# Kernel tuning notes

Hardware: AMD Instinct MI355X
Metric: run time of the kernel (lower is better)

Reference implementation:

```python
import jax, jax.numpy as jnp
import numpy as np

N = 1048576
N_GRID = 256
DX = 1.0 / N_GRID
INV_DX = float(N_GRID)
DT = 2e-5
P_VOL = (DX * 0.5) ** 2
P_RHO = 1.0
P_MASS = P_VOL * P_RHO
E_MOD = 1000.0
NU = 0.2
MU_0 = E_MOD / (2.0 * (1.0 + NU))
LAM_0 = E_MOD * NU / ((1.0 + NU) * (1.0 - 2.0 * NU))
GRAVITY = 50.0


def setup_inputs() -> dict:
    key = jax.random.key(0)
    k = jax.random.split(key, 5)
    x = 0.1 + 0.8 * jax.random.uniform(k[0], (N, 2), dtype=jnp.float32)
    v = 0.1 * jax.random.normal(k[1], (N, 2), dtype=jnp.float32)
    C = 0.5 * jax.random.normal(k[2], (N, 2, 2), dtype=jnp.float32)
    F = jnp.eye(2, dtype=jnp.float32)[None] + 0.1 * jax.random.normal(k[3], (N, 2, 2), dtype=jnp.float32)
    material = jax.random.randint(k[4], (N,), 0, 3, dtype=jnp.int32)
    Jp = jnp.ones((N,), dtype=jnp.float32)
    return {"x": x, "v": v, "C": C, "F": F, "material": material, "Jp": Jp}


def reference(x, v, C, F, material, Jp):
    dt, inv_dx, dx = DT, INV_DX, DX
    base = jnp.floor(x * inv_dx - 0.5).astype(jnp.int32)          # [N,2]
    fx = x * inv_dx - base.astype(x.dtype)                        # [N,2]
    # quadratic B-spline weights, stacked over the 3 taps -> [3,N,2]
    w = jnp.stack([0.5 * (1.5 - fx) ** 2,
                   0.75 - (fx - 1.0) ** 2,
                   0.5 * (fx - 0.5) ** 2], axis=0)

    # deformation gradient update
    F = F + dt * jnp.einsum('nij,njk->nik', C, F)

    h = jnp.exp(10.0 * (1.0 - Jp))
    h = jnp.where(material == 1, 0.3, h)
    mu = jnp.where(material == 0, 0.0, MU_0 * h)
    lam = LAM_0 * h

    # per-particle 2x2 SVD (original pads to 3x3 and slices back)
    U, sig, Vh = jnp.linalg.svd(F)

    # snow plasticity: clamp singular values, track Jp
    clamped = jnp.clip(sig, 1.0 - 2.5e-2, 1.0 + 4.5e-3)
    is_snow = material == 2
    Jp = jnp.where(is_snow, Jp * jnp.prod(sig / clamped, axis=-1), Jp)
    sig = jnp.where(is_snow[:, None], clamped, sig)

    J = jnp.prod(sig, axis=-1)
    eye2 = jnp.eye(2, dtype=x.dtype)
    F_fluid = eye2[None] * jnp.sqrt(J)[:, None, None]             # J^(1/n_dim), n_dim=2
    F_snow = jnp.einsum('nij,nj,njk->nik', U, sig, Vh)
    F = jnp.where((material == 0)[:, None, None], F_fluid,
                  jnp.where(is_snow[:, None, None], F_snow, F))

    R = jnp.einsum('nij,njk->nik', U, Vh)
    stress = (2.0 * mu[:, None, None] * jnp.einsum('nij,nkj->nik', F - R, F)
              + eye2[None] * (lam * J * (J - 1.0))[:, None, None])
    stress = (-dt * P_VOL * 4.0 * inv_dx ** 2) * stress
    affine = stress + P_MASS * C                                   # [N,2,2]

    # ---- P2G scatter over the 3x3 stencil (vectorized over 9 taps) ----
    offs = jnp.array([[i, j] for i in range(3) for j in range(3)], dtype=jnp.int32)  # [9,2]
    weight = w[offs[:, 0], :, 0] * w[offs[:, 1], :, 1]             # [9,N]
    target = base[None, :, :] + offs[:, None, :]                   # [9,N,2]
    idx = target[..., 0] * N_GRID + target[..., 1]                 # [9,N]
    flat_idx = idx.reshape(-1)
    NG2 = N_GRID * N_GRID

    v_add = P_MASS * v - jnp.einsum('nij,nj->ni', affine, x)       # [N,2]
    grid_v = jax.ops.segment_sum((weight[..., None] * v_add[None]).reshape(-1, 2),
                                 flat_idx, num_segments=NG2).reshape(N_GRID, N_GRID, 2)
    grid_affine = jax.ops.segment_sum((weight[..., None, None] * affine[None]).reshape(-1, 4),
                                      flat_idx, num_segments=NG2).reshape(N_GRID, N_GRID, 2, 2)
    grid_m = jax.ops.segment_sum((weight * P_MASS).reshape(-1),
                                 flat_idx, num_segments=NG2).reshape(N_GRID, N_GRID)

    grid_x = jnp.stack(jnp.meshgrid(jnp.arange(N_GRID), jnp.arange(N_GRID), indexing='ij'),
                       axis=-1).astype(x.dtype) * dx               # [G,G,2]
    grid_v = grid_v + jnp.einsum('abij,abj->abi', grid_affine, grid_x)

    # grid ops: momentum -> velocity, gravity, boundary clamps
    m = grid_m[..., None]
    grid_v = jnp.where(m > 0, grid_v / jnp.maximum(m, 1e-12), grid_v)
    grid_v = grid_v.at[:, :, 1].add(-dt * GRAVITY)
    grid_v = grid_v.at[:3, :, 0].max(0.0)
    grid_v = grid_v.at[-2:, :, 0].min(0.0)
    grid_v = grid_v.at[:, :3, 1].max(0.0)
    grid_v = grid_v.at[:, -2:, 1].min(0.0)

    # ---- G2P gather ----
    gvf = grid_v.reshape(NG2, 2)
    g_v = gvf[idx]                                                 # [9,N,2]
    new_v = jnp.sum(weight[..., None] * g_v, axis=0)               # [N,2]
    pos = target.astype(x.dtype) * dx                              # [9,N,2]
    new_C = jnp.sum(weight[..., None, None] * g_v[..., :, None] * pos[..., None, :], axis=0)
    new_C = (new_C - new_v[..., None] * x[:, None, :]) * (4.0 * inv_dx ** 2)

    x = x + dt * new_v
    return (x, new_v, new_C, F, material, Jp)
```

## Files before the change

kernel.cpp:

```cpp
#include <hip/hip_runtime.h>

#define NG 256
#define NG2 (NG*NG)

constexpr float DX      = 1.0f / 256.0f;
constexpr float INV_DX  = 256.0f;
constexpr float DT      = 2e-5f;
constexpr float P_VOL   = (1.0f/512.0f) * (1.0f/512.0f);
constexpr float P_MASS  = P_VOL;
constexpr float MU_0    = 1000.0f / (2.0f * 1.2f);
constexpr float LAM_0   = 1000.0f * 0.2f / (1.2f * 0.6f);
constexpr float GRAV    = 50.0f;

__device__ __forceinline__ int bin_of(float px, float py) {
    int bx = (int)floorf(px * INV_DX - 0.5f);
    int by = (int)floorf(py * INV_DX - 0.5f);
    bx = min(max(bx, 0), NG - 1);
    by = min(max(by, 0), NG - 1);
    return (bx << 8) | by;
}

__device__ __forceinline__ float bw(float t) {
    float at = fabsf(t);
    float a  = fmaxf(1.5f - at, 0.0f);
    float w1 = 0.75f - t * t;
    float w2 = 0.5f * a * a;
    return (at < 0.5f) ? w1 : w2;
}


__global__ __launch_bounds__(256) void binrank_kernel(
    const float* __restrict__ x, int* __restrict__ counts, int* __restrict__ rank, int n)
{
    int i = blockIdx.x * blockDim.x + threadIdx.x;
    if (i >= n) return;
    float2 p = ((const float2*)x)[i];
    int b = bin_of(p.x, p.y);
    rank[i] = atomicAdd(&counts[b], 1);
}

__global__ __launch_bounds__(256) void scan1_kernel(
    const int* __restrict__ counts, int* __restrict__ starts, int* __restrict__ bsum)
{
    __shared__ int tmp[256];
    int t = threadIdx.x, b = blockIdx.x;
    int v = counts[b * 256 + t];
    tmp[t] = v;
    __syncthreads();
    #pragma unroll
    for (int off = 1; off < 256; off <<= 1) {
        int add = (t >= off) ? tmp[t - off] : 0;
        __syncthreads();
        tmp[t] += add;
        __syncthreads();
    }
    starts[b * 256 + t] = tmp[t] - v;
    if (t == 255) bsum[b] = tmp[255];
}

__global__ __launch_bounds__(256) void scan2_kernel(int* __restrict__ bsum)
{
    __shared__ int tmp[256];
    int t = threadIdx.x;
    int v = bsum[t];
    tmp[t] = v;
    __syncthreads();
    #pragma unroll
    for (int off = 1; off < 256; off <<= 1) {
        int add = (t >= off) ? tmp[t - off] : 0;
        __syncthreads();
        tmp[t] += add;
        __syncthreads();
    }
    bsum[t] = tmp[t] - v;
}

__global__ __launch_bounds__(256) void scan3_kernel(
    int* __restrict__ starts, const int* __restrict__ bsum, int n)
{
    int i = blockIdx.x * blockDim.x + threadIdx.x;
    if (i < NG2) starts[i] += bsum[i >> 8];
    if (i == 0) starts[NG2] = n;
}


__device__ __forceinline__ void particle_update(
    int i,
    const float2* __restrict__ x2, const float2* __restrict__ v2,
    const float4* __restrict__ C4, const float4* __restrict__ F4,
    const int* __restrict__ mat, const float* __restrict__ Jp,
    const int* __restrict__ starts, const int* __restrict__ rank,
    float4* __restrict__ srec0, float4* __restrict__ srec1,
    float4* __restrict__ F_out4, float* __restrict__ mat_out, float* __restrict__ Jp_out)
{
    float2 xp = x2[i];
    float2 vp = v2[i];
    float4 Cp = C4[i];
    float4 Fp = F4[i];
    int    m  = mat[i];
    float  jp = Jp[i];

    float px = xp.x, py = xp.y;
    float C00 = Cp.x, C01 = Cp.y, C10 = Cp.z, C11 = Cp.w;
    float a = Fp.x, b = Fp.y, c = Fp.z, d = Fp.w;

    float na = a + DT*(C00*a + C01*c);
    float nb = b + DT*(C00*b + C01*d);
    float nc = c + DT*(C10*a + C11*c);
    float nd = d + DT*(C10*b + C11*d);
    a = na; b = nb; c = nc; d = nd;

    float h = expf(10.0f * (1.0f - jp));
    if (m == 1) h = 0.3f;
    float mu  = (m == 0) ? 0.0f : MU_0 * h;
    float lam = LAM_0 * h;

    float S00 = a*a + c*c, S01 = a*b + c*d, S11 = b*b + d*d;
    float mh = 0.5f*(S00 + S11), dh = 0.5f*(S00 - S11);
    float delta = sqrtf(dh*dh + S01*S01);
    float sig1 = sqrtf(fmaxf(mh + delta, 0.0f));
    float sig2 = sqrtf(fmaxf(mh - delta, 0.0f));
    float e0, e1;
    if (dh >= 0.0f) { e0 = delta + dh; e1 = S01; }
    else            { e0 = S01;        e1 = delta - dh; }
    float elen = sqrtf(e0*e0 + e1*e1);
    float vc, vs;
    if (elen > 1e-30f) { float il = 1.0f/elen; vc = e0*il; vs = e1*il; }
    else               { vc = 1.0f; vs = 0.0f; }
    float inv1 = 1.0f / fmaxf(sig1, 1e-30f);
    float inv2 = 1.0f / fmaxf(sig2, 1e-30f);
    float u1x = ( a*vc + b*vs) * inv1, u1y = ( c*vc + d*vs) * inv1;
    float u2x = (-a*vs + b*vc) * inv2, u2y = (-c*vs + d*vc) * inv2;

    if (m == 2) {
        float c1 = fminf(fmaxf(sig1, 1.0f - 2.5e-2f), 1.0f + 4.5e-3f);
        float c2 = fminf(fmaxf(sig2, 1.0f - 2.5e-2f), 1.0f + 4.5e-3f);
        jp = jp * (sig1 / c1) * (sig2 / c2);
        sig1 = c1; sig2 = c2;
    }
    float J = sig1 * sig2;

    if (m == 0) {
        float s = sqrtf(J);
        a = s; b = 0.0f; c = 0.0f; d = s;
    } else if (m == 2) {
        a = sig1*u1x*vc - sig2*u2x*vs;
        b = sig1*u1x*vs + sig2*u2x*vc;
        c = sig1*u1y*vc - sig2*u2y*vs;
        d = sig1*u1y*vs + sig2*u2y*vc;
    }
    float R00 = u1x*vc - u2x*vs, R01 = u1x*vs + u2x*vc;
    float R10 = u1y*vc - u2y*vs, R11 = u1y*vs + u2y*vc;

    float k2mu = 2.0f * mu;
    float fr00 = a - R00, fr01 = b - R01, fr10 = c - R10, fr11 = d - R11;
    float ljj  = lam * J * (J - 1.0f);
    float st00 = k2mu*(fr00*a + fr01*b) + ljj;
    float st01 = k2mu*(fr00*c + fr01*d);
    float st10 = k2mu*(fr10*a + fr11*b);
    float st11 = k2mu*(fr10*c + fr11*d) + ljj;
    const float coef = -DT * P_VOL * 4.0f * INV_DX * INV_DX;
    float A00 = coef*st00 + P_MASS*C00;
    float A01 = coef*st01 + P_MASS*C01;
    float A10 = coef*st10 + P_MASS*C10;
    float A11 = coef*st11 + P_MASS*C11;

    float bx_ = P_MASS*vp.x - (A00*px + A01*py);
    float by_ = P_MASS*vp.y - (A10*px + A11*py);

    int bidx = bin_of(px, py);
    int sidx = starts[bidx] + rank[i];
    srec0[sidx] = make_float4(px * INV_DX, py * INV_DX, bx_, by_);
    srec1[sidx] = make_float4(A00, A01, A10, A11);

    F_out4[i]  = make_float4(a, b, c, d);
    mat_out[i] = (float)m;
    Jp_out[i]  = jp;
}

__global__ __launch_bounds__(256) void compute_scatter_kernel(
    const float* __restrict__ x, const float* __restrict__ v,
    const float* __restrict__ C, const float* __restrict__ F,
    const int* __restrict__ mat, const float* __restrict__ Jp,
    const int* __restrict__ starts, const int* __restrict__ rank,
    float4* __restrict__ srec0, float4* __restrict__ srec1,
    float* __restrict__ F_out, float* __restrict__ mat_out, float* __restrict__ Jp_out,
    int n)
{
    int t = blockIdx.x * blockDim.x + threadIdx.x;
    int half = n >> 1;
    const float2* x2 = (const float2*)x;
    const float2* v2 = (const float2*)v;
    const float4* C4 = (const float4*)C;
    const float4* F4 = (const float4*)F;
    float4* F_out4 = (float4*)F_out;

    if (t < half) {
        particle_update(t,        x2, v2, C4, F4, mat, Jp, starts, rank,
                        srec0, srec1, F_out4, mat_out, Jp_out);
        particle_update(t + half, x2, v2, C4, F4, mat, Jp, starts, rank,
                        srec0, srec1, F_out4, mat_out, Jp_out);
    } else if ((n & 1) && t == half) {
        particle_update(n - 1, x2, v2, C4, F4, mat, Jp, starts, rank,
                        srec0, srec1, F_out4, mat_out, Jp_out);
    }
}

__global__ __launch_bounds__(256) void gather_grid_kernel(
    const float4* __restrict__ srec0, const float4* __restrict__ srec1,
    const int* __restrict__ starts, float2* __restrict__ gv)
{
    int gtid  = blockIdx.x * blockDim.x + threadIdx.x;
    int cell  = gtid >> 3;
    int slice = gtid & 7;
    int gi = cell >> 8, gj = cell & (NG - 1);

    float fgi = (float)gi, fgj = (float)gj;
    float posx = fgi * DX, posy = fgj * DX;
    float msum = 0.0f, mvx = 0.0f, mvy = 0.0f;

    int i0 = max(gi - 2, 0);
    int j0 = max(gj - 2, 0);

    for (int bi = i0; bi <= gi; ++bi) {
        int row = bi << 8;
        int s = starts[row + j0];
        int e = starts[row + gj + 1];
        for (int k = s + slice; k < e; k += 16) {
            float4 r0 = srec0[k];
            float4 r1 = srec1[k];
            int k2 = k + 8;
            bool sec = (k2 < e);
            float4 q0, q1;
            if (sec) { q0 = srec0[k2]; q1 = srec1[k2]; }
            float w = bw(r0.x - fgi) * bw(r0.y - fgj);
            msum += w;
            mvx  += w * (r0.z + r1.x * posx + r1.y * posy);
            mvy  += w * (r0.w + r1.z * posx + r1.w * posy);
            if (sec) {
                float w2 = bw(q0.x - fgi) * bw(q0.y - fgj);
                msum += w2;
                mvx  += w2 * (q0.z + q1.x * posx + q1.y * posy);
                mvy  += w2 * (q0.w + q1.z * posx + q1.w * posy);
            }
        }
    }

    #pragma unroll
    for (int off = 1; off < 8; off <<= 1) {
        msum += __shfl_xor(msum, off);
        mvx  += __shfl_xor(mvx,  off);
        mvy  += __shfl_xor(mvy,  off);
    }

    if (slice == 0) {
        float mass = msum * P_MASS;
        float vx = mvx, vy = mvy;
        if (mass > 0.0f) {
            float im = 1.0f / fmaxf(mass, 1e-12f);
            vx *= im; vy *= im;
        }
        vy -= DT * GRAV;
        if (gi < 3)      vx = fmaxf(vx, 0.0f);
        if (gi >= NG-2)  vx = fminf(vx, 0.0f);
        if (gj < 3)      vy = fmaxf(vy, 0.0f);
        if (gj >= NG-2)  vy = fminf(vy, 0.0f);
        gv[cell] = make_float2(vx, vy);
    }
}

__global__ __launch_bounds__(256) void g2p_kernel(
    const float* __restrict__ x, const float2* __restrict__ gv,
    float* __restrict__ x_out, float* __restrict__ v_out, float* __restrict__ C_out,
    int n)
{
    int i = blockIdx.x * blockDim.x + threadIdx.x;
    if (i >= n) return;

    float2 xp = ((const float2*)x)[i];
    float px = xp.x, py = xp.y;
    float bxf = floorf(px * INV_DX - 0.5f), byf = floorf(py * INV_DX - 0.5f);
    float fx = px * INV_DX - bxf, fy = py * INV_DX - byf;
    float wxs[3] = { 0.5f*(1.5f-fx)*(1.5f-fx), 0.75f-(fx-1.0f)*(fx-1.0f), 0.5f*(fx-0.5f)*(fx-0.5f) };
    float wys[3] = { 0.5f*(1.5f-fy)*(1.5f-fy), 0.75f-(fy-1.0f)*(fy-1.0f), 0.5f*(fy-0.5f)*(fy-0.5f) };
    int bix = (int)bxf, biy = (int)byf;

    float nvx = 0.0f, nvy = 0.0f;
    float c00 = 0.0f, c01 = 0.0f, c10 = 0.0f, c11 = 0.0f;
    #pragma unroll
    for (int ii = 0; ii < 3; ++ii) {
        float posx = (bxf + (float)ii) * DX;
        int rowbase = (bix + ii) * NG + biy;
        #pragma unroll
        for (int jj = 0; jj < 3; ++jj) {
            float w = wxs[ii] * wys[jj];
            float posy = (byf + (float)jj) * DX;
            float2 g = gv[rowbase + jj];
            nvx += w * g.x; nvy += w * g.y;
            c00 += w * g.x * posx; c01 += w * g.x * posy;
            c10 += w * g.y * posx; c11 += w * g.y * posy;
        }
    }
    const float K = 4.0f * INV_DX * INV_DX;
    c00 = (c00 - nvx * px) * K; c01 = (c01 - nvx * py) * K;
    c10 = (c10 - nvy * px) * K; c11 = (c11 - nvy * py) * K;

    ((float2*)x_out)[i] = make_float2(px + DT * nvx, py + DT * nvy);
    ((float2*)v_out)[i] = make_float2(nvx, nvy);
    ((float4*)C_out)[i] = make_float4(c00, c01, c10, c11);
}

extern "C" void kernel_launch(void* const* d_in, const int* in_sizes, int n_in,
                              void* d_out, int out_size, void* d_ws, size_t ws_size,
                              hipStream_t stream) {
    const float* x   = (const float*)d_in[0];
    const float* v   = (const float*)d_in[1];
    const float* C   = (const float*)d_in[2];
    const float* F   = (const float*)d_in[3];
    const int*   mat = (const int*)d_in[4];
    const float* Jp  = (const float*)d_in[5];

    int n = in_sizes[0] / 2;

    float* out     = (float*)d_out;
    float* x_out   = out;
    float* v_out   = out + (size_t)2*n;
    float* C_out   = out + (size_t)4*n;
    float* F_out   = out + (size_t)8*n;
    float* mat_out = out + (size_t)12*n;
    float* Jp_out  = out + (size_t)13*n;

    int blocks = (n + 255) / 256;

    char* ws = (char*)d_ws;
    size_t off = 0;
    int* counts = (int*)(ws + off); off += (size_t)NG2 * 4;
    int* starts = (int*)(ws + off); off += (size_t)(NG2 + 1) * 4;
    int* bsum   = (int*)(ws + off); off += 256 * 4;
    int* rank   = (int*)(ws + off); off += (size_t)n * 4;
    off = (off + 15) & ~(size_t)15;
    float4* srec0 = (float4*)(ws + off); off += (size_t)n * 16;
    float4* srec1 = (float4*)(ws + off); off += (size_t)n * 16;
    float2* gv    = (float2*)(ws + off); off += (size_t)NG2 * 8;

    hipMemsetAsync(counts, 0, (size_t)NG2 * 4, stream);
    binrank_kernel<<<blocks, 256, 0, stream>>>(x, counts, rank, n);
    scan1_kernel<<<NG2/256, 256, 0, stream>>>(counts, starts, bsum);
    scan2_kernel<<<1, 256, 0, stream>>>(bsum);
    scan3_kernel<<<NG2/256, 256, 0, stream>>>(starts, bsum, n);
    int half_blocks = ((n + 1) / 2 + 255) / 256;
    compute_scatter_kernel<<<half_blocks, 256, 0, stream>>>(x, v, C, F, mat, Jp,
                                                            starts, rank, srec0, srec1,
                                                            F_out, mat_out, Jp_out, n);
    gather_grid_kernel<<<(NG2*8)/256, 256, 0, stream>>>(srec0, srec1, starts, gv);
    g2p_kernel<<<blocks, 256, 0, stream>>>(x, gv, x_out, v_out, C_out, n);
}
```

Baseline: 147.7 us.

## Tile grid gather with LDS-staged particle records and index permutation

The compute kernel now writes per-particle payloads coalesced in particle order, storing them in the output buffer, and scatters only a 4-byte index into a sorted permutation instead of two scattered 16-byte records. The grid gather is restructured into 8x4 cell tiles, each of which stages every particle record from its 10x7-bin halo into LDS once and then reuses it across cells, with a global-memory fallback when a tile holds more than CAP particles. This trades scattered writes and repeated global reads for an indirect gather through perm and a large LDS footprint that limits occupancy. It also drops the two-particles-per-thread layout in the compute kernel.

```diff
diff --git a/kernel.cpp b/kernel.cpp
--- a/kernel.cpp
+++ b/kernel.cpp
@@ -2,6 +2,12 @@
 
 #define NG 256
 #define NG2 (NG*NG)
+
+#define TI 8
+#define TJ 4
+#define NTILES ((NG/TI)*(NG/TJ))
+#define CAP 2048
+#define RSTRIDE 9
 
 constexpr float DX      = 1.0f / 256.0f;
 constexpr float INV_DX  = 256.0f;
@@ -84,19 +90,23 @@
 }
 
 
-__device__ __forceinline__ void particle_update(
-    int i,
-    const float2* __restrict__ x2, const float2* __restrict__ v2,
-    const float4* __restrict__ C4, const float4* __restrict__ F4,
+__global__ __launch_bounds__(256) void compute_kernel(
+    const float* __restrict__ x, const float* __restrict__ v,
+    const float* __restrict__ C, const float* __restrict__ F,
     const int* __restrict__ mat, const float* __restrict__ Jp,
     const int* __restrict__ starts, const int* __restrict__ rank,
-    float4* __restrict__ srec0, float4* __restrict__ srec1,
-    float4* __restrict__ F_out4, float* __restrict__ mat_out, float* __restrict__ Jp_out)
-{
-    float2 xp = x2[i];
-    float2 vp = v2[i];
-    float4 Cp = C4[i];
-    float4 Fp = F4[i];
+    float4* __restrict__ payload0, float4* __restrict__ payload1,
+    int* __restrict__ perm,
+    float4* __restrict__ F_out4, float* __restrict__ mat_out, float* __restrict__ Jp_out,
+    int n)
+{
+    int i = blockIdx.x * blockDim.x + threadIdx.x;
+    if (i >= n) return;
+
+    float2 xp = ((const float2*)x)[i];
+    float2 vp = ((const float2*)v)[i];
+    float4 Cp = ((const float4*)C)[i];
+    float4 Fp = ((const float4*)F)[i];
     int    m  = mat[i];
     float  jp = Jp[i];
 
@@ -168,80 +178,112 @@
     float bx_ = P_MASS*vp.x - (A00*px + A01*py);
     float by_ = P_MASS*vp.y - (A10*px + A11*py);
 
-    int bidx = bin_of(px, py);
-    int sidx = starts[bidx] + rank[i];
-    srec0[sidx] = make_float4(px * INV_DX, py * INV_DX, bx_, by_);
-    srec1[sidx] = make_float4(A00, A01, A10, A11);
+    payload0[i] = make_float4(px * INV_DX, py * INV_DX, bx_, by_);
+    payload1[i] = make_float4(A00, A01, A10, A11);
+
+    int sidx = starts[bin_of(px, py)] + rank[i];
+    perm[sidx] = i;
 
     F_out4[i]  = make_float4(a, b, c, d);
     mat_out[i] = (float)m;
     Jp_out[i]  = jp;
 }
 
-__global__ __launch_bounds__(256) void compute_scatter_kernel(
-    const float* __restrict__ x, const float* __restrict__ v,
-    const float* __restrict__ C, const float* __restrict__ F,
-    const int* __restrict__ mat, const float* __restrict__ Jp,
-    const int* __restrict__ starts, const int* __restrict__ rank,
-    float4* __restrict__ srec0, float4* __restrict__ srec1,
-    float* __restrict__ F_out, float* __restrict__ mat_out, float* __restrict__ Jp_out,
-    int n)
-{
-    int t = blockIdx.x * blockDim.x + threadIdx.x;
-    int half = n >> 1;
-    const float2* x2 = (const float2*)x;
-    const float2* v2 = (const float2*)v;
-    const float4* C4 = (const float4*)C;
-    const float4* F4 = (const float4*)F;
-    float4* F_out4 = (float4*)F_out;
-
-    if (t < half) {
-        particle_update(t,        x2, v2, C4, F4, mat, Jp, starts, rank,
-                        srec0, srec1, F_out4, mat_out, Jp_out);
-        particle_update(t + half, x2, v2, C4, F4, mat, Jp, starts, rank,
-                        srec0, srec1, F_out4, mat_out, Jp_out);
-    } else if ((n & 1) && t == half) {
-        particle_update(n - 1, x2, v2, C4, F4, mat, Jp, starts, rank,
-                        srec0, srec1, F_out4, mat_out, Jp_out);
-    }
-}
-
-__global__ __launch_bounds__(256) void gather_grid_kernel(
-    const float4* __restrict__ srec0, const float4* __restrict__ srec1,
-    const int* __restrict__ starts, float2* __restrict__ gv)
-{
-    int gtid  = blockIdx.x * blockDim.x + threadIdx.x;
-    int cell  = gtid >> 3;
-    int slice = gtid & 7;
-    int gi = cell >> 8, gj = cell & (NG - 1);
-
+
+__global__ __launch_bounds__(256) void gather_tile_kernel(
+    const float4* __restrict__ payload0, const float4* __restrict__ payload1,
+    const int* __restrict__ perm, const int* __restrict__ starts,
+    float2* __restrict__ gv)
+{
+    __shared__ float lds[CAP * RSTRIDE];
+    __shared__ int stable[10][7];
+    __shared__ int rowbase[10];
+    __shared__ int total_s;
+
+    int bid = blockIdx.x;
+    int swz = (bid & 7) * (NTILES / 8) + (bid >> 3);
+    int ti = swz >> 6;
+    int tj = swz & 63;
+    int t  = threadIdx.x;
+
+    int r0 = ti * TI;
+    int c0 = tj * TJ;
+
+    if (t < 70) {
+        int r = t / 7, u = t % 7;
+        int br = r0 - 2 + r;
+        int col = c0 - 2 + u;
+        int val = 0;
+        if (br >= 0 && br < NG) {
+            int cc = col < 0 ? 0 : col;
+            val = starts[br * NG + cc];
+        }
+        stable[r][u] = val;
+    }
+    __syncthreads();
+    if (t == 0) {
+        int run = 0;
+        #pragma unroll
+        for (int r = 0; r < 10; ++r) {
+            rowbase[r] = run;
+            run += stable[r][6] - stable[r][0];
+        }
+        total_s = run;
+    }
+    __syncthreads();
+    bool use_lds = (total_s <= CAP);
+
+    if (use_lds) {
+        #pragma unroll 1
+        for (int r = 0; r < 10; ++r) {
+            int s = stable[r][0], e = stable[r][6];
+            int base = rowbase[r];
+            for (int k = s + t; k < e; k += 256) {
+                int i = perm[k];
+                float4 p0 = payload0[i];
+                float4 p1 = payload1[i];
+                int slot = (base + (k - s)) * RSTRIDE;
+                lds[slot+0] = p0.x; lds[slot+1] = p0.y;
+                lds[slot+2] = p0.z; lds[slot+3] = p0.w;
+                lds[slot+4] = p1.x; lds[slot+5] = p1.y;
+                lds[slot+6] = p1.z; lds[slot+7] = p1.w;
+            }
+        }
+        __syncthreads();
+    }
+
+    int cell  = t >> 3;
+    int slice = t & 7;
+    int ci = cell >> 2;
+    int cj = cell & 3;
+    int gi = r0 + ci, gj = c0 + cj;
     float fgi = (float)gi, fgj = (float)gj;
     float posx = fgi * DX, posy = fgj * DX;
     float msum = 0.0f, mvx = 0.0f, mvy = 0.0f;
 
-    int i0 = max(gi - 2, 0);
-    int j0 = max(gj - 2, 0);
-
-    for (int bi = i0; bi <= gi; ++bi) {
-        int row = bi << 8;
-        int s = starts[row + j0];
-        int e = starts[row + gj + 1];
-        for (int k = s + slice; k < e; k += 16) {
-            float4 r0 = srec0[k];
-            float4 r1 = srec1[k];
-            int k2 = k + 8;
-            bool sec = (k2 < e);
-            float4 q0, q1;
-            if (sec) { q0 = srec0[k2]; q1 = srec1[k2]; }
-            float w = bw(r0.x - fgi) * bw(r0.y - fgj);
-            msum += w;
-            mvx  += w * (r0.z + r1.x * posx + r1.y * posy);
-            mvy  += w * (r0.w + r1.z * posx + r1.w * posy);
-            if (sec) {
-                float w2 = bw(q0.x - fgi) * bw(q0.y - fgj);
-                msum += w2;
-                mvx  += w2 * (q0.z + q1.x * posx + q1.y * posy);
-                mvy  += w2 * (q0.w + q1.z * posx + q1.w * posy);
+    #pragma unroll
+    for (int dr = 0; dr < 3; ++dr) {
+        int r = ci + dr;
+        int a = stable[r][cj];
+        int b = stable[r][cj + 3];
+        if (use_lds) {
+            int base = rowbase[r] - stable[r][0];
+            for (int k = a + slice; k < b; k += 8) {
+                const float* rec = &lds[(base + k) * RSTRIDE];
+                float w = bw(rec[0] - fgi) * bw(rec[1] - fgj);
+                msum += w;
+                mvx  += w * (rec[2] + rec[4] * posx + rec[5] * posy);
+                mvy  += w * (rec[3] + rec[6] * posx + rec[7] * posy);
+            }
+        } else {
+            for (int k = a + slice; k < b; k += 8) {
+                int i = perm[k];
+                float4 p0 = payload0[i];
+                float4 p1 = payload1[i];
+                float w = bw(p0.x - fgi) * bw(p0.y - fgj);
+                msum += w;
+                mvx  += w * (p0.z + p1.x * posx + p1.y * posy);
+                mvy  += w * (p0.w + p1.z * posx + p1.w * posy);
             }
         }
     }
@@ -261,11 +303,11 @@
             vx *= im; vy *= im;
         }
         vy -= DT * GRAV;
-        if (gi < 3)      vx = fmaxf(vx, 0.0f);
-        if (gi >= NG-2)  vx = fminf(vx, 0.0f);
-        if (gj < 3)      vy = fmaxf(vy, 0.0f);
-        if (gj >= NG-2)  vy = fminf(vy, 0.0f);
-        gv[cell] = make_float2(vx, vy);
+        if (gi < 3)       vx = fmaxf(vx, 0.0f);
+        if (gi >= NG-2)   vx = fminf(vx, 0.0f);
+        if (gj < 3)       vy = fmaxf(vy, 0.0f);
+        if (gj >= NG-2)   vy = fminf(vy, 0.0f);
+        gv[gi * NG + gj] = make_float2(vx, vy);
     }
 }
 
@@ -330,6 +372,9 @@
     float* mat_out = out + (size_t)12*n;
     float* Jp_out  = out + (size_t)13*n;
 
+    float4* payload0 = (float4*)out;
+    float4* payload1 = (float4*)(out + (size_t)4*n);
+
     int blocks = (n + 255) / 256;
 
     char* ws = (char*)d_ws;
@@ -338,20 +383,19 @@
     int* starts = (int*)(ws + off); off += (size_t)(NG2 + 1) * 4;
     int* bsum   = (int*)(ws + off); off += 256 * 4;
     int* rank   = (int*)(ws + off); off += (size_t)n * 4;
+    int* perm   = (int*)(ws + off); off += (size_t)n * 4;
     off = (off + 15) & ~(size_t)15;
-    float4* srec0 = (float4*)(ws + off); off += (size_t)n * 16;
-    float4* srec1 = (float4*)(ws + off); off += (size_t)n * 16;
-    float2* gv    = (float2*)(ws + off); off += (size_t)NG2 * 8;
+    float2* gv  = (float2*)(ws + off); off += (size_t)NG2 * 8;
 
     hipMemsetAsync(counts, 0, (size_t)NG2 * 4, stream);
     binrank_kernel<<<blocks, 256, 0, stream>>>(x, counts, rank, n);
     scan1_kernel<<<NG2/256, 256, 0, stream>>>(counts, starts, bsum);
     scan2_kernel<<<1, 256, 0, stream>>>(bsum);
     scan3_kernel<<<NG2/256, 256, 0, stream>>>(starts, bsum, n);
-    int half_blocks = ((n + 1) / 2 + 255) / 256;
-    compute_scatter_kernel<<<half_blocks, 256, 0, stream>>>(x, v, C, F, mat, Jp,
-                                                            starts, rank, srec0, srec1,
-                                                            F_out, mat_out, Jp_out, n);
-    gather_grid_kernel<<<(NG2*8)/256, 256, 0, stream>>>(srec0, srec1, starts, gv);
+    compute_kernel<<<blocks, 256, 0, stream>>>(x, v, C, F, mat, Jp,
+                                               starts, rank,
+                                               payload0, payload1, perm,
+                                               (float4*)F_out, mat_out, Jp_out, n);
+    gather_tile_kernel<<<NTILES, 256, 0, stream>>>(payload0, payload1, perm, starts, gv);
     g2p_kernel<<<blocks, 256, 0, stream>>>(x, gv, x_out, v_out, C_out, n);
 }
```

Result: slower. 180.2 us (+22.1%).
